# Kernel tuning notes

Measured on AMD Instinct MI355X. Metric: run time of the kernel, lower is better.

Reference implementation:

```python
import jax, jax.numpy as jnp
import numpy as np

N_GRAPHS = 50
EPS = 1e-5
N_NODES, N_EDGES, F, L, N_HEADS = 50000, 800000, 64, 3, 3


def _bn(x, gamma, beta):
    # BatchNorm1d over nodes, training-mode (biased batch statistics)
    m = x.mean(axis=0)
    v = jnp.mean((x - m) ** 2, axis=0)
    return gamma * (x - m) * jax.lax.rsqrt(v + EPS) + beta


def _pna_layer(x, src, dst, preW, preb, postW, postb, linW, linb, avg_log, avg_lin):
    N = x.shape[0]
    # pre-MLP on concatenated (target x_i, source x_j): [E, 2F] -> [E, F]
    h = jnp.concatenate([x[dst], x[src]], axis=-1) @ preW + preb
    ones = jnp.ones((h.shape[0],), h.dtype)
    cnt = jax.ops.segment_sum(ones, dst, num_segments=N)[:, None]
    has = cnt > 0
    deg = jnp.maximum(cnt, 1.0)  # PNAConv clamps degree to >= 1
    mean = jax.ops.segment_sum(h, dst, num_segments=N) / deg
    mean2 = jax.ops.segment_sum(h * h, dst, num_segments=N) / deg
    std = jnp.sqrt(jax.nn.relu(mean2 - mean * mean) + EPS)
    mn = jnp.where(has, jax.ops.segment_min(h, dst, num_segments=N), 0.0)
    mx = jnp.where(has, jax.ops.segment_max(h, dst, num_segments=N), 0.0)
    aggr = jnp.concatenate([mean, mn, mx, std], axis=-1)  # [N, 4F]
    log_deg = jnp.log(deg + 1.0)
    out = jnp.concatenate([aggr,
                           aggr * (log_deg / avg_log),   # amplification
                           aggr * (avg_log / log_deg),   # attenuation
                           aggr * (deg / avg_lin)],      # linear
                          axis=-1)                       # [N, 16F]
    out = jnp.concatenate([x, out], axis=-1) @ postW + postb  # post-MLP [N, F]
    return out @ linW + linb


def _forward(x, deg_hist, preW, preb, postW, postb, linW, linb, bn_g, bn_b,
             sharedW, sharedb, hW1, hb1, hW2, hb2, hW3, hb3, src, dst, batch):
    bins = jnp.arange(deg_hist.shape[0], dtype=deg_hist.dtype)
    tot = deg_hist.sum()
    avg_lin = (bins * deg_hist).sum() / tot
    avg_log = (jnp.log(bins + 1.0) * deg_hist).sum() / tot
    for l in range(preW.shape[0]):  # only num_conv_layers convs run (zip truncation)
        x = _pna_layer(x, src, dst, preW[l], preb[l], postW[l], postb[l],
                       linW[l], linb[l], avg_log, avg_lin)
        x = jax.nn.relu(_bn(x, bn_g[l], bn_b[l]))
    gcnt = jax.ops.segment_sum(jnp.ones((x.shape[0],), x.dtype), batch,
                               num_segments=N_GRAPHS)[:, None]
    g = jax.ops.segment_sum(x, batch, num_segments=N_GRAPHS) / jnp.maximum(gcnt, 1.0)
    g = jax.nn.relu(g @ sharedW + sharedb)  # shared MLP (num_shared=1)
    h1 = jax.nn.relu(jnp.einsum('gd,hdk->hgk', g, hW1) + hb1[:, None, :])
    h2 = jax.nn.relu(jnp.einsum('hgk,hkm->hgm', h1, hW2) + hb2[:, None, :])
    o = jnp.einsum('hgm,hmo->hgo', h2, hW3) + hb3[:, None, :]  # [H, G, 1]
    return jnp.transpose(o[..., 0])  # [G, H] == torch.cat(head outputs, dim=1)


def setup_inputs():
    key = jax.random.key(0)
    ks = jax.random.split(key, 12)

    def w(k, shape, fan_in):
        return jax.random.normal(k, shape, jnp.float32) / np.sqrt(fan_in)

    return {
        "x": jax.random.normal(ks[0], (N_NODES, F), jnp.float32),
        "edge_index": jax.random.randint(ks[1], (2, N_EDGES), 0, N_NODES),
        "batch": jnp.sort(jax.random.randint(ks[2], (N_NODES,), 0, N_GRAPHS)),
        "deg_hist": jax.random.uniform(ks[3], (33,), jnp.float32) + 0.01,
        "preW": w(ks[4], (L, 2 * F, F), 2 * F),
        "preb": jnp.zeros((L, F), jnp.float32),
        "postW": w(ks[5], (L, 17 * F, F), 17 * F),
        "postb": jnp.zeros((L, F), jnp.float32),
        "linW": w(ks[6], (L, F, F), F),
        "linb": jnp.zeros((L, F), jnp.float32),
        "bn_g": jnp.ones((L, F), jnp.float32),
        "bn_b": jnp.zeros((L, F), jnp.float32),
        "sharedW": w(ks[7], (F, F), F),
        "sharedb": jnp.zeros((F,), jnp.float32),
        "hW1": w(ks[8], (N_HEADS, F, 50), F),
        "hb1": jnp.zeros((N_HEADS, 50), jnp.float32),
        "hW2": w(ks[9], (N_HEADS, 50, 25), 50),
        "hb2": jnp.zeros((N_HEADS, 25), jnp.float32),
        "hW3": w(ks[10], (N_HEADS, 25, 1), 25),
        "hb3": jnp.zeros((N_HEADS, 1), jnp.float32),
    }


def reference(x, edge_index, batch, deg_hist, preW, preb, postW, postb,
              linW, linb, bn_g, bn_b, sharedW, sharedb,
              hW1, hb1, hW2, hb2, hW3, hb3):
    return _forward(x, deg_hist, preW, preb, postW, postb, linW, linb,
                    bn_g, bn_b, sharedW, sharedb, hW1, hb1, hW2, hb2,
                    hW3, hb3, edge_index[0], edge_index[1], batch)
```

## Files before the change

### kernel.cpp

```cpp
#include <hip/hip_runtime.h>
#include <math.h>

#define N_NODES 50000
#define N_EDGES 800000
#define NGRAPHS 50
#define NHEADS 3
#define EPS 1e-5f
#define NPASS 8
#define PASS_W ((N_NODES + NPASS - 1) / NPASS)

typedef _Float16 half8 __attribute__((ext_vector_type(8)));
typedef float f32x4 __attribute__((ext_vector_type(4)));

__global__ void __launch_bounds__(256) k_zero_setup(int* cnt, int* cur, float* gsum, float* gcnt,
                                                    float* part, float* partq,
                                                    const float* dh, int nbins, float* scal) {
  int gid = blockIdx.x * 256 + threadIdx.x;
  int gs = gridDim.x * 256;
  for (int i = gid; i < N_NODES; i += gs) { cnt[i] = 0; cur[i] = 0; }
  for (int i = gid; i < NGRAPHS * 64; i += gs) gsum[i] = 0.f;
  for (int i = gid; i < NGRAPHS; i += gs) gcnt[i] = 0.f;
  for (int i = gid; i < 128 * 64; i += gs) { part[i] = 0.f; partq[i] = 0.f; }
  if (blockIdx.x == 0 && threadIdx.x < 64) {
    int t = threadIdx.x;
    float v = (t < nbins) ? dh[t] : 0.f;
    float lv = logf((float)t + 1.f) * v;
    float bv = (float)t * v;
    for (int d = 32; d > 0; d >>= 1) {
      v  += __shfl_down(v,  d, 64);
      lv += __shfl_down(lv, d, 64);
      bv += __shfl_down(bv, d, 64);
    }
    if (t == 0) { scal[0] = lv / v; scal[1] = bv / v; }
  }
}

__global__ void __launch_bounds__(256) k_hist(const int* __restrict__ dst, int* __restrict__ cnt) {
  int e = blockIdx.x * 256 + threadIdx.x;
  if (e < N_EDGES) atomicAdd(&cnt[dst[e]], 1);
}

__global__ void __launch_bounds__(256) k_scan_a(const int* __restrict__ cnt, int* __restrict__ off,
                                                int* __restrict__ blksum) {
  __shared__ int lds[256];
  int t = threadIdx.x;
  int base = blockIdx.x * 1024 + t * 4;
  int v0 = (base + 0 < N_NODES) ? cnt[base + 0] : 0;
  int v1 = (base + 1 < N_NODES) ? cnt[base + 1] : 0;
  int v2 = (base + 2 < N_NODES) ? cnt[base + 2] : 0;
  int v3 = (base + 3 < N_NODES) ? cnt[base + 3] : 0;
  int tsum = v0 + v1 + v2 + v3;
  lds[t] = tsum; __syncthreads();
  for (int d = 1; d < 256; d <<= 1) {
    int x = (t >= d) ? lds[t - d] : 0;
    __syncthreads();
    lds[t] += x;
    __syncthreads();
  }
  int run = lds[t] - tsum;
  if (base + 0 < N_NODES) off[base + 0] = run; run += v0;
  if (base + 1 < N_NODES) off[base + 1] = run; run += v1;
  if (base + 2 < N_NODES) off[base + 2] = run; run += v2;
  if (base + 3 < N_NODES) off[base + 3] = run;
  if (t == 255) blksum[blockIdx.x] = lds[255];
}

__global__ void __launch_bounds__(64) k_scan_b(const int* __restrict__ blksum, int* __restrict__ blkoff) {
  int t = threadIdx.x;
  int own = (t < 49) ? blksum[t] : 0;
  int v = own;
  for (int d = 1; d < 64; d <<= 1) {
    int u = __shfl_up(v, d, 64);
    if (t >= d) v += u;
  }
  if (t < 49) blkoff[t] = v - own;
}

__global__ void __launch_bounds__(256) k_scan_c(int* __restrict__ off, const int* __restrict__ blkoff) {
  int i = blockIdx.x * 256 + threadIdx.x;
  if (i < N_NODES) off[i] += blkoff[i >> 10];
  if (i == 0) off[N_NODES] = N_EDGES;
}

__global__ void __launch_bounds__(256) k_scatter(const int* __restrict__ src, const int* __restrict__ dst,
                                                 const int* __restrict__ off, int* __restrict__ cur,
                                                 int* __restrict__ esrc) {
  int e = blockIdx.x * 256 + threadIdx.x;
  if (e >= N_EDGES) return;
  int d = dst[e];
  int sv = src[e] << 7;
  #pragma unroll 1
  for (int p = 0; p < NPASS; ++p) {
    int lo = p * PASS_W;
    if (d >= lo && d < lo + PASS_W) {
      int pos = off[d] + atomicAdd(&cur[d], 1);
      esrc[pos] = sv;
    }
  }
}

__global__ void __launch_bounds__(256) k_prep(const float* __restrict__ xin, _Float16* __restrict__ xout,
                                              const float* __restrict__ preW, const float* __restrict__ postW,
                                              const float* __restrict__ linW, _Float16* __restrict__ preP,
                                              _Float16* __restrict__ postAP, _Float16* __restrict__ postBP,
                                              _Float16* __restrict__ linP) {
  int t0 = blockIdx.x * 256 + threadIdx.x;
  if (t0 < 400000) {
    const float* s = xin + (size_t)t0 * 8;
    float4 v0 = *(const float4*)s;
    float4 v1 = *(const float4*)(s + 4);
    half8 h = {(_Float16)v0.x, (_Float16)v0.y, (_Float16)v0.z, (_Float16)v0.w,
               (_Float16)v1.x, (_Float16)v1.y, (_Float16)v1.z, (_Float16)v1.w};
    *(half8*)(xout + (size_t)t0 * 8) = h;
    return;
  }
  int t = t0 - 400000;
  if (t < 24576) {
    int l = t >> 13, r = t & 8191;
    int j = r & 7, lane = (r >> 3) & 63, ctg = (r >> 9) & 7, kc = r >> 12;
    int k = kc * 32 + ((lane >> 4) << 3) + j;
    int col = ctg * 16 + (lane & 15);
    const float* W = preW + (size_t)l * 8192;
    float v = (col < 64) ? W[k * 64 + col] : W[(64 + k) * 64 + (col - 64)];
    preP[(size_t)l * 8192 + r] = (_Float16)v;
  } else if (t < 221184) {
    int q = t - 24576;
    int l = q >> 16, r = q & 65535;
    int j = r & 7, lane = (r >> 3) & 63, ct = (r >> 9) & 3, s = (r >> 11) & 3, kc = r >> 13;
    int k = kc * 32 + ((lane >> 4) << 3) + j;
    int col = ct * 16 + (lane & 15);
    postAP[(size_t)l * 65536 + r] = (_Float16)postW[(size_t)l * 69632 + (size_t)(64 + s * 256 + k) * 64 + col];
  } else if (t < 233472) {
    int q = t - 221184;
    int l = q >> 12, r = q & 4095;
    int j = r & 7, lane = (r >> 3) & 63, ct = (r >> 9) & 3, kc = r >> 11;
    int k = kc * 32 + ((lane >> 4) << 3) + j;
    int col = ct * 16 + (lane & 15);
    postBP[(size_t)l * 4096 + r] = (_Float16)postW[(size_t)l * 69632 + (size_t)k * 64 + col];
  } else if (t < 245760) {
    int q = t - 233472;
    int l = q >> 12, r = q & 4095;
    int j = r & 7, lane = (r >> 3) & 63, ct = (r >> 9) & 3, kc = r >> 11;
    int k = kc * 32 + ((lane >> 4) << 3) + j;
    int col = ct * 16 + (lane & 15);
    linP[(size_t)l * 4096 + r] = (_Float16)linW[(size_t)l * 4096 + (size_t)k * 64 + col];
  }
}

__global__ void __launch_bounds__(256) k_mfma_g1(const _Float16* __restrict__ yin, const float* __restrict__ bnsc,
                                                 const float* __restrict__ bnsh, int applyBN,
                                                 const _Float16* __restrict__ wp, const float* __restrict__ bias,
                                                 _Float16* __restrict__ Aout, _Float16* __restrict__ Bout,
                                                 _Float16* __restrict__ xout) {
  int t = threadIdx.x, lane = t & 63, wave = t >> 6;
  int r0 = blockIdx.x * 64;
  int mrow = lane & 15, q8 = ((lane >> 4) << 3);
  f32x4 acc[4][2];
  #pragma unroll
  for (int rt = 0; rt < 4; ++rt) { acc[rt][0] = (f32x4)0.f; acc[rt][1] = (f32x4)0.f; }
  #pragma unroll
  for (int kc = 0; kc < 2; ++kc) {
    int k0 = kc * 32 + q8;
    half8 a[4];
    #pragma unroll
    for (int rt = 0; rt < 4; ++rt) {
      int r = min(r0 + rt * 16 + mrow, N_NODES - 1);
      a[rt] = *(const half8*)(yin + (size_t)r * 64 + k0);
    }
    if (applyBN) {
      float4 sc0 = *(const float4*)(bnsc + k0);
      float4 sc1 = *(const float4*)(bnsc + k0 + 4);
      float4 sh0 = *(const float4*)(bnsh + k0);
      float4 sh1 = *(const float4*)(bnsh + k0 + 4);
      #pragma unroll
      for (int rt = 0; rt < 4; ++rt) {
        half8 v = a[rt];
        v[0] = (_Float16)fmaxf((float)v[0] * sc0.x + sh0.x, 0.f);
        v[1] = (_Float16)fmaxf((float)v[1] * sc0.y + sh0.y, 0.f);
        v[2] = (_Float16)fmaxf((float)v[2] * sc0.z + sh0.z, 0.f);
        v[3] = (_Float16)fmaxf((float)v[3] * sc0.w + sh0.w, 0.f);
        v[4] = (_Float16)fmaxf((float)v[4] * sc1.x + sh1.x, 0.f);
        v[5] = (_Float16)fmaxf((float)v[5] * sc1.y + sh1.y, 0.f);
        v[6] = (_Float16)fmaxf((float)v[6] * sc1.z + sh1.z, 0.f);
        v[7] = (_Float16)fmaxf((float)v[7] * sc1.w + sh1.w, 0.f);
        a[rt] = v;
      }
      if (wave == 0) {
        #pragma unroll
        for (int rt = 0; rt < 4; ++rt) {
          int r = min(r0 + rt * 16 + mrow, N_NODES - 1);
          *(half8*)(xout + (size_t)r * 64 + k0) = a[rt];
        }
      }
    }
    #pragma unroll
    for (int ci = 0; ci < 2; ++ci) {
      int ctg = wave * 2 + ci;
      half8 b = *(const half8*)(wp + (size_t)((kc * 8 + ctg) * 64 + lane) * 8);
      #pragma unroll
      for (int rt = 0; rt < 4; ++rt)
        acc[rt][ci] = __builtin_amdgcn_mfma_f32_16x16x32_f16(a[rt], b, acc[rt][ci], 0, 0, 0);
    }
  }
  #pragma unroll
  for (int ci = 0; ci < 2; ++ci) {
    int col = (wave * 2 + ci) * 16 + mrow;
    bool isA = col < 64;
    float bv = isA ? bias[col] : 0.f;
    _Float16* outp = isA ? (Aout + col) : (Bout + (col - 64));
    #pragma unroll
    for (int rt = 0; rt < 4; ++rt)
      #pragma unroll
      for (int reg = 0; reg < 4; ++reg) {
        int row = r0 + rt * 16 + ((lane >> 4) << 2) + reg;
        if (row < N_NODES) outp[(size_t)row * 64] = (_Float16)(acc[rt][ci][reg] + bv);
      }
  }
}

__global__ void __launch_bounds__(256) k_aggr(const _Float16* __restrict__ A, const _Float16* __restrict__ B,
                                              const int* __restrict__ off, const int* __restrict__ esrc,
                                              const float* __restrict__ scal, _Float16* __restrict__ aggr,
                                              float4* __restrict__ scales) {
  int wave = threadIdx.x >> 6, lane = threadIdx.x & 63;
  int n = blockIdx.x * 4 + wave;
  float c = (float)A[(size_t)n * 64 + lane];
  int e0 = __builtin_amdgcn_readfirstlane(off[n]);
  int e1 = __builtin_amdgcn_readfirstlane(off[n + 1]);
  int deg = e1 - e0;
  const char* Bb = (const char*)B;
  int lo2 = lane * 2;
  float sum = 0.f, sq = 0.f, mn = 3.4e38f, mx = -3.4e38f;
  int e = e0;
  for (; e + 3 < e1; e += 4) {
    int r0 = __builtin_amdgcn_readfirstlane(esrc[e]);
    int r1 = __builtin_amdgcn_readfirstlane(esrc[e + 1]);
    int r2 = __builtin_amdgcn_readfirstlane(esrc[e + 2]);
    int r3 = __builtin_amdgcn_readfirstlane(esrc[e + 3]);
    float b0 = (float)*(const _Float16*)(Bb + r0 + lo2);
    float b1 = (float)*(const _Float16*)(Bb + r1 + lo2);
    float b2 = (float)*(const _Float16*)(Bb + r2 + lo2);
    float b3 = (float)*(const _Float16*)(Bb + r3 + lo2);
    sum += (b0 + b1) + (b2 + b3);
    sq += b0 * b0; sq += b1 * b1; sq += b2 * b2; sq += b3 * b3;
    mn = fminf(mn, fminf(fminf(b0, b1), fminf(b2, b3)));
    mx = fmaxf(mx, fmaxf(fmaxf(b0, b1), fmaxf(b2, b3)));
  }
  for (; e < e1; ++e) {
    int r = __builtin_amdgcn_readfirstlane(esrc[e]);
    float b = (float)*(const _Float16*)(Bb + r + lo2);
    sum += b; sq += b * b; mn = fminf(mn, b); mx = fmaxf(mx, b);
  }
  _Float16* arow = aggr + (size_t)n * 256;
  if (deg == 0) {
    arow[lane] = (_Float16)0.f; arow[64 + lane] = (_Float16)0.f;
    arow[128 + lane] = (_Float16)0.f; arow[192 + lane] = (_Float16)sqrtf(EPS);
  } else {
    float inv = 1.f / (float)deg;
    float mb = sum * inv, m2 = sq * inv;
    float var = fmaxf(m2 - mb * mb, 0.f);
    arow[lane]       = (_Float16)(c + mb);
    arow[64 + lane]  = (_Float16)(c + mn);
    arow[128 + lane] = (_Float16)(c + mx);
    arow[192 + lane] = (_Float16)sqrtf(var + EPS);
  }
  if (lane == 0) {
    float degf = fmaxf((float)deg, 1.f);
    float ld = logf(degf + 1.f);
    float al = scal[0], av = scal[1];
    scales[n] = make_float4(ld / al, al / ld, degf / av, 0.f);
  }
}

__global__ void __launch_bounds__(256) k_mfma_g2(const _Float16* __restrict__ aggr, const _Float16* __restrict__ x16,
                                                 const _Float16* __restrict__ wpA, const _Float16* __restrict__ wpB,
                                                 const float* __restrict__ postb, const float4* __restrict__ scales,
                                                 _Float16* __restrict__ ybuf) {
  int t = threadIdx.x, lane = t & 63, ct = t >> 6;
  int r0 = blockIdx.x * 64;
  int mrow = lane & 15, q8 = ((lane >> 4) << 3);
  f32x4 acc[4][4];
  #pragma unroll
  for (int rt = 0; rt < 4; ++rt)
    #pragma unroll
    for (int s = 0; s < 4; ++s) acc[rt][s] = (f32x4)0.f;
  #pragma unroll 2
  for (int kc = 0; kc < 8; ++kc) {
    half8 a[4];
    #pragma unroll
    for (int rt = 0; rt < 4; ++rt) {
      int r = min(r0 + rt * 16 + mrow, N_NODES - 1);
      a[rt] = *(const half8*)(aggr + (size_t)r * 256 + kc * 32 + q8);
    }
    #pragma unroll
    for (int s = 0; s < 4; ++s) {
      half8 b = *(const half8*)(wpA + (size_t)((((kc * 4 + s) * 4 + ct) * 64) + lane) * 8);
      #pragma unroll
      for (int rt = 0; rt < 4; ++rt)
        acc[rt][s] = __builtin_amdgcn_mfma_f32_16x16x32_f16(a[rt], b, acc[rt][s], 0, 0, 0);
    }
  }
  #pragma unroll
  for (int kc = 0; kc < 2; ++kc) {
    half8 a[4];
    #pragma unroll
    for (int rt = 0; rt < 4; ++rt) {
      int r = min(r0 + rt * 16 + mrow, N_NODES - 1);
      a[rt] = *(const half8*)(x16 + (size_t)r * 64 + kc * 32 + q8);
    }
    half8 b = *(const half8*)(wpB + (size_t)(((kc * 4 + ct) * 64) + lane) * 8);
    #pragma unroll
    for (int rt = 0; rt < 4; ++rt)
      acc[rt][0] = __builtin_amdgcn_mfma_f32_16x16x32_f16(a[rt], b, acc[rt][0], 0, 0, 0);
  }
  int col = ct * 16 + mrow;
  float pb = postb[col];
  #pragma unroll
  for (int rt = 0; rt < 4; ++rt)
    #pragma unroll
    for (int reg = 0; reg < 4; ++reg) {
      int row = r0 + rt * 16 + ((lane >> 4) << 2) + reg;
      if (row < N_NODES) {
        float4 sc = scales[row];
        float v = acc[rt][0][reg] + sc.x * acc[rt][1][reg] + sc.y * acc[rt][2][reg] + sc.z * acc[rt][3][reg] + pb;
        ybuf[(size_t)row * 64 + col] = (_Float16)v;
      }
    }
}

__global__ void __launch_bounds__(256) k_mfma_g3(const _Float16* __restrict__ yin, const _Float16* __restrict__ wp,
                                                 const float* __restrict__ bias, _Float16* __restrict__ y16,
                                                 float* __restrict__ part, float* __restrict__ partq) {
  int t = threadIdx.x, lane = t & 63, ct = t >> 6;
  int r0 = blockIdx.x * 64;
  int mrow = lane & 15, q8 = ((lane >> 4) << 3);
  f32x4 acc[4];
  #pragma unroll
  for (int rt = 0; rt < 4; ++rt) acc[rt] = (f32x4)0.f;
  #pragma unroll
  for (int kc = 0; kc < 2; ++kc) {
    half8 a[4];
    #pragma unroll
    for (int rt = 0; rt < 4; ++rt) {
      int r = min(r0 + rt * 16 + mrow, N_NODES - 1);
      a[rt] = *(const half8*)(yin + (size_t)r * 64 + kc * 32 + q8);
    }
    half8 b = *(const half8*)(wp + (size_t)(((kc * 4 + ct) * 64) + lane) * 8);
    #pragma unroll
    for (int rt = 0; rt < 4; ++rt)
      acc[rt] = __builtin_amdgcn_mfma_f32_16x16x32_f16(a[rt], b, acc[rt], 0, 0, 0);
  }
  int col = ct * 16 + mrow;
  float bv = bias[col];
  float s = 0.f, q = 0.f;
  #pragma unroll
  for (int rt = 0; rt < 4; ++rt)
    #pragma unroll
    for (int reg = 0; reg < 4; ++reg) {
      int row = r0 + rt * 16 + ((lane >> 4) << 2) + reg;
      if (row < N_NODES) {
        float v = acc[rt][reg] + bv;
        y16[(size_t)row * 64 + col] = (_Float16)v;
        s += v; q += v * v;
      }
    }
  int slot = (blockIdx.x & 127) * 64 + col;
  atomicAdd(&part[slot], s);
  atomicAdd(&partq[slot], q);
}

__global__ void __launch_bounds__(256) k_bnfinal(float* __restrict__ part, float* __restrict__ partq,
                                                 const float* __restrict__ g, const float* __restrict__ b,
                                                 float* __restrict__ scale, float* __restrict__ shift) {
  __shared__ float ls[256], lq[256];
  int t = threadIdx.x, col = t & 63, qtr = t >> 6;
  float s = 0.f, q = 0.f;
  for (int i = 0; i < 32; ++i) {
    int slot = qtr * 32 + i;
    s += part[slot * 64 + col];
    q += partq[slot * 64 + col];
  }
  ls[t] = s; lq[t] = q; __syncthreads();
  if (t < 64) {
    s = ls[t] + ls[64 + t] + ls[128 + t] + ls[192 + t];
    q = lq[t] + lq[64 + t] + lq[128 + t] + lq[192 + t];
    float m = s / (float)N_NODES;
    float v = fmaxf(q / (float)N_NODES - m * m, 0.f);
    float sc = g[t] * rsqrtf(v + EPS);
    scale[t] = sc;
    shift[t] = b[t] - m * sc;
  }
  __syncthreads();
  for (int i = t; i < 128 * 64; i += 256) { part[i] = 0.f; partq[i] = 0.f; }
}

__global__ void __launch_bounds__(256) k_pool(const _Float16* __restrict__ y16, const float* __restrict__ bnsc,
                                              const float* __restrict__ bnsh, const int* __restrict__ batch,
                                              float* __restrict__ gsum, float* __restrict__ gcnt) {
  int t = threadIdx.x, col = t & 63, rl = t >> 6;
  float sc = bnsc[col], sh = bnsh[col];
  int rbeg = blockIdx.x * 64 + rl * 16;
  int rend = min(rbeg + 16, N_NODES);
  int curg = -1, cr = 0;
  float acc = 0.f;
  for (int r = rbeg; r < rend; ++r) {
    int g = batch[r];
    if (g != curg) {
      if (curg >= 0) {
        atomicAdd(&gsum[curg * 64 + col], acc);
        if (col == 0) atomicAdd(&gcnt[curg], (float)cr);
      }
      curg = g; acc = 0.f; cr = 0;
    }
    acc += fmaxf((float)y16[(size_t)r * 64 + col] * sc + sh, 0.f); cr++;
  }
  if (curg >= 0) {
    atomicAdd(&gsum[curg * 64 + col], acc);
    if (col == 0) atomicAdd(&gcnt[curg], (float)cr);
  }
}

__global__ void __launch_bounds__(64) k_shared(const float* __restrict__ gsum, const float* __restrict__ gcnt,
                                               const float* __restrict__ W, const float* __restrict__ b,
                                               float* __restrict__ g2) {
  __shared__ float gm[64];
  int g = blockIdx.x, j = threadIdx.x;
  float cv = fmaxf(gcnt[g], 1.f);
  gm[j] = gsum[g * 64 + j] / cv;
  __syncthreads();
  float s = b[j];
  for (int k = 0; k < 64; ++k) s += gm[k] * W[k * 64 + j];
  g2[g * 64 + j] = fmaxf(s, 0.f);
}

__global__ void __launch_bounds__(64) k_heads(const float* __restrict__ g2, const float* __restrict__ hW1,
                                              const float* __restrict__ hb1, const float* __restrict__ hW2,
                                              const float* __restrict__ hb2, const float* __restrict__ hW3,
                                              const float* __restrict__ hb3, float* __restrict__ out) {
  __shared__ float gv[64], h1[50], h2[25];
  int bid = blockIdx.x;
  int g = bid / NHEADS, h = bid % NHEADS;
  int t = threadIdx.x;
  gv[t] = g2[g * 64 + t];
  __syncthreads();
  if (t < 50) {
    float s = hb1[h * 50 + t];
    for (int k = 0; k < 64; ++k) s += gv[k] * hW1[h * 3200 + k * 50 + t];
    h1[t] = fmaxf(s, 0.f);
  }
  __syncthreads();
  if (t < 25) {
    float s = hb2[h * 25 + t];
    for (int k = 0; k < 50; ++k) s += h1[k] * hW2[h * 1250 + k * 25 + t];
    h2[t] = fmaxf(s, 0.f);
  }
  __syncthreads();
  if (t == 0) {
    float s = hb3[h];
    for (int k = 0; k < 25; ++k) s += h2[k] * hW3[h * 25 + k];
    out[g * NHEADS + h] = s;
  }
}

extern "C" void kernel_launch(void* const* d_in, const int* in_sizes, int n_in,
                              void* d_out, int out_size, void* d_ws, size_t ws_size,
                              hipStream_t stream) {
  const float* x0    = (const float*)d_in[0];
  const int*   eidx  = (const int*)d_in[1];
  const int*   batch = (const int*)d_in[2];
  const float* dh    = (const float*)d_in[3];
  const float* preW  = (const float*)d_in[4];
  const float* preb  = (const float*)d_in[5];
  const float* postW = (const float*)d_in[6];
  const float* postb = (const float*)d_in[7];
  const float* linW  = (const float*)d_in[8];
  const float* linb  = (const float*)d_in[9];
  const float* bng   = (const float*)d_in[10];
  const float* bnb   = (const float*)d_in[11];
  const float* shW   = (const float*)d_in[12];
  const float* shb   = (const float*)d_in[13];
  const float* hW1   = (const float*)d_in[14];
  const float* hb1   = (const float*)d_in[15];
  const float* hW2   = (const float*)d_in[16];
  const float* hb2   = (const float*)d_in[17];
  const float* hW3   = (const float*)d_in[18];
  const float* hb3   = (const float*)d_in[19];
  float* out = (float*)d_out;

  char* ws = (char*)d_ws;
  size_t o = 0;
  auto alloc = [&](size_t bytes) {
    char* p = ws + o;
    o = (o + bytes + 255) & ~(size_t)255;
    return p;
  };
  float* scal   = (float*)alloc(8 * 4);
  int* off      = (int*)alloc((N_NODES + 1) * 4);
  int* cnt      = (int*)alloc(N_NODES * 4);
  int* cur      = (int*)alloc(N_NODES * 4);
  int* esrc     = (int*)alloc(N_EDGES * 4);
  int* blks     = (int*)alloc(64 * 4);
  int* blko     = (int*)alloc(64 * 4);
  _Float16* A16    = (_Float16*)alloc((size_t)N_NODES * 64 * 2 + 256 * 16);
  _Float16* B16    = (_Float16*)alloc((size_t)N_NODES * 64 * 2 + 256 * 16);
  _Float16* aggr16 = (_Float16*)alloc((size_t)50048 * 256 * 2);
  _Float16* x16a   = (_Float16*)alloc((size_t)N_NODES * 64 * 2 + 256 * 16);
  _Float16* xbuf   = (_Float16*)alloc((size_t)N_NODES * 64 * 2 + 256 * 16);
  _Float16* ybuf16 = (_Float16*)alloc((size_t)N_NODES * 64 * 2 + 256 * 16);
  _Float16* y16    = (_Float16*)alloc((size_t)N_NODES * 64 * 2 + 256 * 16);
  float4* scales = (float4*)alloc((size_t)N_NODES * 16);
  _Float16* preP   = (_Float16*)alloc(3 * 8192 * 2);
  _Float16* postAP = (_Float16*)alloc((size_t)3 * 65536 * 2);
  _Float16* postBP = (_Float16*)alloc(3 * 4096 * 2);
  _Float16* linP   = (_Float16*)alloc(3 * 4096 * 2);
  float* part   = (float*)alloc(128 * 64 * 4);
  float* partq  = (float*)alloc(128 * 64 * 4);
  float* bnsc   = (float*)alloc(64 * 4);
  float* bnsh   = (float*)alloc(64 * 4);
  float* gsum   = (float*)alloc(NGRAPHS * 64 * 4);
  float* gcnt   = (float*)alloc(NGRAPHS * 4);
  float* g2b    = (float*)alloc(NGRAPHS * 64 * 4);

  const int* srcv = eidx;
  const int* dstv = eidx + N_EDGES;

  k_zero_setup<<<256, 256, 0, stream>>>(cnt, cur, gsum, gcnt, part, partq, dh, in_sizes[3], scal);
  k_hist<<<(N_EDGES + 255) / 256, 256, 0, stream>>>(dstv, cnt);
  k_scan_a<<<49, 256, 0, stream>>>(cnt, off, blks);
  k_scan_b<<<1, 64, 0, stream>>>(blks, blko);
  k_scan_c<<<196, 256, 0, stream>>>(off, blko);
  k_scatter<<<(N_EDGES + 255) / 256, 256, 0, stream>>>(srcv, dstv, off, cur, esrc);
  k_prep<<<(400000 + 245760 + 255) / 256, 256, 0, stream>>>(x0, x16a, preW, postW, linW,
                                                            preP, postAP, postBP, linP);

  for (int l = 0; l < 3; ++l) {
    const _Float16* g1in = (l == 0) ? x16a : y16;
    const _Float16* xc   = (l == 0) ? x16a : xbuf;
    k_mfma_g1<<<782, 256, 0, stream>>>(g1in, bnsc, bnsh, (l > 0) ? 1 : 0,
                                       preP + (size_t)l * 8192, preb + l * 64, A16, B16, xbuf);
    k_aggr<<<12500, 256, 0, stream>>>(A16, B16, off, esrc, scal, aggr16, scales);
    k_mfma_g2<<<782, 256, 0, stream>>>(aggr16, xc, postAP + (size_t)l * 65536, postBP + (size_t)l * 4096,
                                       postb + l * 64, scales, ybuf16);
    k_mfma_g3<<<782, 256, 0, stream>>>(ybuf16, linP + (size_t)l * 4096, linb + l * 64, y16, part, partq);
    k_bnfinal<<<1, 256, 0, stream>>>(part, partq, bng + l * 64, bnb + l * 64, bnsc, bnsh);
  }
  k_pool<<<782, 256, 0, stream>>>(y16, bnsc, bnsh, batch, gsum, gcnt);
  k_shared<<<NGRAPHS, 64, 0, stream>>>(gsum, gcnt, shW, shb, g2b);
  k_heads<<<NGRAPHS * NHEADS, 64, 0, stream>>>(g2b, hW1, hb1, hW2, hb2, hW3, hb3, out);
}
```

Measured before the change: 501.8 us.

## Fuse aggregation into post-MLP GEMM, two-level CSR partition, merge head kernels

Three changes land together. The edge-to-CSR scatter, which used 8 passes of global atomics, becomes a two-stage partition: edges are first binned into 256-node windows through per-block shared-memory histograms, then each window is sorted locally in LDS before being written out. The per-node aggregation kernel is fused into the post-MLP MFMA kernel, so the aggregate rows and degree scalers stay in shared memory and never round-trip through global memory. The shared-MLP and head kernels are merged into one launch. The cost is fewer aggregation waves in flight (782 blocks, each wave handling 16 nodes serially instead of one node per wave) and extra workspace for the partition buffers.

```diff
diff --git a/kernel.cpp b/kernel.cpp
--- a/kernel.cpp
+++ b/kernel.cpp
@@ -6,18 +6,18 @@
 #define NGRAPHS 50
 #define NHEADS 3
 #define EPS 1e-5f
-#define NPASS 8
-#define PASS_W ((N_NODES + NPASS - 1) / NPASS)
+#define NWIN 196
+#define WSH 8
 
 typedef _Float16 half8 __attribute__((ext_vector_type(8)));
 typedef float f32x4 __attribute__((ext_vector_type(4)));
 
-__global__ void __launch_bounds__(256) k_zero_setup(int* cnt, int* cur, float* gsum, float* gcnt,
+__global__ void __launch_bounds__(256) k_zero_setup(int* cnt, float* gsum, float* gcnt,
                                                     float* part, float* partq,
                                                     const float* dh, int nbins, float* scal) {
   int gid = blockIdx.x * 256 + threadIdx.x;
   int gs = gridDim.x * 256;
-  for (int i = gid; i < N_NODES; i += gs) { cnt[i] = 0; cur[i] = 0; }
+  for (int i = gid; i < N_NODES; i += gs) cnt[i] = 0;
   for (int i = gid; i < NGRAPHS * 64; i += gs) gsum[i] = 0.f;
   for (int i = gid; i < NGRAPHS; i += gs) gcnt[i] = 0.f;
   for (int i = gid; i < 128 * 64; i += gs) { part[i] = 0.f; partq[i] = 0.f; }
@@ -76,25 +76,102 @@
   if (t < 49) blkoff[t] = v - own;
 }
 
-__global__ void __launch_bounds__(256) k_scan_c(int* __restrict__ off, const int* __restrict__ blkoff) {
+__global__ void __launch_bounds__(256) k_scan_c(int* __restrict__ off, const int* __restrict__ blkoff,
+                                                int* __restrict__ wincur) {
   int i = blockIdx.x * 256 + threadIdx.x;
-  if (i < N_NODES) off[i] += blkoff[i >> 10];
+  if (i < N_NODES) {
+    int fo = off[i] + blkoff[i >> 10];
+    off[i] = fo;
+    if ((i & 255) == 0) wincur[i >> WSH] = fo;
+  }
   if (i == 0) off[N_NODES] = N_EDGES;
 }
 
-__global__ void __launch_bounds__(256) k_scatter(const int* __restrict__ src, const int* __restrict__ dst,
-                                                 const int* __restrict__ off, int* __restrict__ cur,
-                                                 int* __restrict__ esrc) {
-  int e = blockIdx.x * 256 + threadIdx.x;
-  if (e >= N_EDGES) return;
-  int d = dst[e];
-  int sv = src[e] << 7;
-  #pragma unroll 1
-  for (int p = 0; p < NPASS; ++p) {
-    int lo = p * PASS_W;
-    if (d >= lo && d < lo + PASS_W) {
-      int pos = off[d] + atomicAdd(&cur[d], 1);
-      esrc[pos] = sv;
+__global__ void __launch_bounds__(256) k_part1(const int* __restrict__ src, const int* __restrict__ dst,
+                                               int* __restrict__ wincur, int* __restrict__ pairS,
+                                               unsigned char* __restrict__ pairDL) {
+  __shared__ int hist[256];
+  __shared__ int scan[256];
+  __shared__ int baseg[256];
+  __shared__ int place[256];
+  __shared__ int sS[2048];
+  __shared__ unsigned char sDL[2048];
+  __shared__ unsigned char sW[2048];
+  int t = threadIdx.x;
+  int base = blockIdx.x * 2048;
+  hist[t] = 0;
+  __syncthreads();
+  int d[8], s[8];
+  #pragma unroll
+  for (int i = 0; i < 8; ++i) {
+    int e = base + t + 256 * i;
+    bool val = e < N_EDGES;
+    d[i] = val ? dst[e] : -1;
+    s[i] = val ? src[e] : 0;
+    if (val) atomicAdd(&hist[d[i] >> WSH], 1);
+  }
+  __syncthreads();
+  int v = hist[t];
+  scan[t] = v; __syncthreads();
+  for (int dd = 1; dd < 256; dd <<= 1) {
+    int x = (t >= dd) ? scan[t - dd] : 0;
+    __syncthreads();
+    scan[t] += x;
+    __syncthreads();
+  }
+  place[t] = scan[t] - v;
+  if (v > 0) baseg[t] = atomicAdd(&wincur[t], v);
+  __syncthreads();
+  #pragma unroll
+  for (int i = 0; i < 8; ++i) {
+    if (d[i] >= 0) {
+      int w = d[i] >> WSH;
+      int p = atomicAdd(&place[w], 1);
+      sS[p] = s[i] << 7;
+      sDL[p] = (unsigned char)(d[i] & 255);
+      sW[p] = (unsigned char)w;
+    }
+  }
+  __syncthreads();
+  int tot = min(N_EDGES - base, 2048);
+  for (int i = t; i < tot; i += 256) {
+    int w = sW[i];
+    int gidx = baseg[w] + (i - (scan[w] - hist[w]));
+    pairS[gidx] = sS[i];
+    pairDL[gidx] = sDL[i];
+  }
+}
+
+__global__ void __launch_bounds__(256) k_part2(const int* __restrict__ off, const int* __restrict__ pairS,
+                                               const unsigned char* __restrict__ pairDL,
+                                               int* __restrict__ esrc) {
+  __shared__ int curW[256];
+  __shared__ int offW[257];
+  __shared__ int esrcW[6144];
+  int w = blockIdx.x, t = threadIdx.x;
+  int n0 = w << WSH;
+  offW[t] = off[min(n0 + t, N_NODES)];
+  if (t == 0) offW[256] = off[min(n0 + 256, N_NODES)];
+  curW[t] = 0;
+  __syncthreads();
+  int start = offW[0];
+  int end = offW[256];
+  int cnt = end - start;
+  if (cnt <= 6144) {
+    for (int i = t; i < cnt; i += 256) {
+      int s = pairS[start + i];
+      int dl = pairDL[start + i];
+      int pos = offW[dl] - start + atomicAdd(&curW[dl], 1);
+      esrcW[pos] = s;
+    }
+    __syncthreads();
+    for (int i = t; i < cnt; i += 256) esrc[start + i] = esrcW[i];
+  } else {
+    for (int i = t; i < cnt; i += 256) {
+      int s = pairS[start + i];
+      int dl = pairDL[start + i];
+      int pos = offW[dl] + atomicAdd(&curW[dl], 1);
+      esrc[pos] = s;
     }
   }
 }
@@ -218,66 +295,75 @@
   }
 }
 
-__global__ void __launch_bounds__(256) k_aggr(const _Float16* __restrict__ A, const _Float16* __restrict__ B,
-                                              const int* __restrict__ off, const int* __restrict__ esrc,
-                                              const float* __restrict__ scal, _Float16* __restrict__ aggr,
-                                              float4* __restrict__ scales) {
-  int wave = threadIdx.x >> 6, lane = threadIdx.x & 63;
-  int n = blockIdx.x * 4 + wave;
-  float c = (float)A[(size_t)n * 64 + lane];
-  int e0 = __builtin_amdgcn_readfirstlane(off[n]);
-  int e1 = __builtin_amdgcn_readfirstlane(off[n + 1]);
-  int deg = e1 - e0;
+__global__ void __launch_bounds__(256) k_aggr_g2(const _Float16* __restrict__ A, const _Float16* __restrict__ B,
+                                                 const int* __restrict__ off, const int* __restrict__ esrc,
+                                                 const float* __restrict__ scal, const _Float16* __restrict__ x16,
+                                                 const _Float16* __restrict__ wpA, const _Float16* __restrict__ wpB,
+                                                 const float* __restrict__ postb, _Float16* __restrict__ ybuf) {
+  __shared__ _Float16 aggrS[64][264];
+  __shared__ float sclS[64][4];
+  int t = threadIdx.x, lane = t & 63, wave = t >> 6;
+  int r0 = blockIdx.x * 64;
+  float al = scal[0], av = scal[1];
   const char* Bb = (const char*)B;
   int lo2 = lane * 2;
-  float sum = 0.f, sq = 0.f, mn = 3.4e38f, mx = -3.4e38f;
-  int e = e0;
-  for (; e + 3 < e1; e += 4) {
-    int r0 = __builtin_amdgcn_readfirstlane(esrc[e]);
-    int r1 = __builtin_amdgcn_readfirstlane(esrc[e + 1]);
-    int r2 = __builtin_amdgcn_readfirstlane(esrc[e + 2]);
-    int r3 = __builtin_amdgcn_readfirstlane(esrc[e + 3]);
-    float b0 = (float)*(const _Float16*)(Bb + r0 + lo2);
-    float b1 = (float)*(const _Float16*)(Bb + r1 + lo2);
-    float b2 = (float)*(const _Float16*)(Bb + r2 + lo2);
-    float b3 = (float)*(const _Float16*)(Bb + r3 + lo2);
-    sum += (b0 + b1) + (b2 + b3);
-    sq += b0 * b0; sq += b1 * b1; sq += b2 * b2; sq += b3 * b3;
-    mn = fminf(mn, fminf(fminf(b0, b1), fminf(b2, b3)));
-    mx = fmaxf(mx, fmaxf(fmaxf(b0, b1), fmaxf(b2, b3)));
-  }
-  for (; e < e1; ++e) {
-    int r = __builtin_amdgcn_readfirstlane(esrc[e]);
-    float b = (float)*(const _Float16*)(Bb + r + lo2);
-    sum += b; sq += b * b; mn = fminf(mn, b); mx = fmaxf(mx, b);
-  }
-  _Float16* arow = aggr + (size_t)n * 256;
-  if (deg == 0) {
-    arow[lane] = (_Float16)0.f; arow[64 + lane] = (_Float16)0.f;
-    arow[128 + lane] = (_Float16)0.f; arow[192 + lane] = (_Float16)sqrtf(EPS);
-  } else {
-    float inv = 1.f / (float)deg;
-    float mb = sum * inv, m2 = sq * inv;
-    float var = fmaxf(m2 - mb * mb, 0.f);
-    arow[lane]       = (_Float16)(c + mb);
-    arow[64 + lane]  = (_Float16)(c + mn);
-    arow[128 + lane] = (_Float16)(c + mx);
-    arow[192 + lane] = (_Float16)sqrtf(var + EPS);
-  }
-  if (lane == 0) {
-    float degf = fmaxf((float)deg, 1.f);
-    float ld = logf(degf + 1.f);
-    float al = scal[0], av = scal[1];
-    scales[n] = make_float4(ld / al, al / ld, degf / av, 0.f);
-  }
-}
-
-__global__ void __launch_bounds__(256) k_mfma_g2(const _Float16* __restrict__ aggr, const _Float16* __restrict__ x16,
-                                                 const _Float16* __restrict__ wpA, const _Float16* __restrict__ wpB,
-                                                 const float* __restrict__ postb, const float4* __restrict__ scales,
-                                                 _Float16* __restrict__ ybuf) {
-  int t = threadIdx.x, lane = t & 63, ct = t >> 6;
-  int r0 = blockIdx.x * 64;
+  for (int i = 0; i < 16; ++i) {
+    int nl = wave * 16 + i;
+    int n = r0 + nl;
+    float c = 0.f;
+    int e0 = 0, e1 = 0;
+    if (n < N_NODES) {
+      c = (float)A[(size_t)n * 64 + lane];
+      e0 = off[n]; e1 = off[n + 1];
+    }
+    e0 = __builtin_amdgcn_readfirstlane(e0);
+    e1 = __builtin_amdgcn_readfirstlane(e1);
+    int deg = e1 - e0;
+    float sum = 0.f, sq = 0.f, mn = 3.4e38f, mx = -3.4e38f;
+    int e = e0;
+    for (; e + 3 < e1; e += 4) {
+      int b0o = __builtin_amdgcn_readfirstlane(esrc[e]);
+      int b1o = __builtin_amdgcn_readfirstlane(esrc[e + 1]);
+      int b2o = __builtin_amdgcn_readfirstlane(esrc[e + 2]);
+      int b3o = __builtin_amdgcn_readfirstlane(esrc[e + 3]);
+      float b0 = (float)*(const _Float16*)(Bb + b0o + lo2);
+      float b1 = (float)*(const _Float16*)(Bb + b1o + lo2);
+      float b2 = (float)*(const _Float16*)(Bb + b2o + lo2);
+      float b3 = (float)*(const _Float16*)(Bb + b3o + lo2);
+      sum += (b0 + b1) + (b2 + b3);
+      sq += b0 * b0; sq += b1 * b1; sq += b2 * b2; sq += b3 * b3;
+      mn = fminf(mn, fminf(fminf(b0, b1), fminf(b2, b3)));
+      mx = fmaxf(mx, fmaxf(fmaxf(b0, b1), fmaxf(b2, b3)));
+    }
+    for (; e < e1; ++e) {
+      int ro = __builtin_amdgcn_readfirstlane(esrc[e]);
+      float b = (float)*(const _Float16*)(Bb + ro + lo2);
+      sum += b; sq += b * b; mn = fminf(mn, b); mx = fmaxf(mx, b);
+    }
+    if (deg == 0) {
+      aggrS[nl][lane] = (_Float16)0.f;
+      aggrS[nl][64 + lane] = (_Float16)0.f;
+      aggrS[nl][128 + lane] = (_Float16)0.f;
+      aggrS[nl][192 + lane] = (_Float16)sqrtf(EPS);
+    } else {
+      float inv = 1.f / (float)deg;
+      float mb = sum * inv, m2 = sq * inv;
+      float var = fmaxf(m2 - mb * mb, 0.f);
+      aggrS[nl][lane]       = (_Float16)(c + mb);
+      aggrS[nl][64 + lane]  = (_Float16)(c + mn);
+      aggrS[nl][128 + lane] = (_Float16)(c + mx);
+      aggrS[nl][192 + lane] = (_Float16)sqrtf(var + EPS);
+    }
+    if (lane == 0) {
+      float degf = fmaxf((float)deg, 1.f);
+      float ld = logf(degf + 1.f);
+      sclS[nl][0] = ld / al;
+      sclS[nl][1] = al / ld;
+      sclS[nl][2] = degf / av;
+    }
+  }
+  __syncthreads();
+  int ct = wave;
   int mrow = lane & 15, q8 = ((lane >> 4) << 3);
   f32x4 acc[4][4];
   #pragma unroll
@@ -288,10 +374,8 @@
   for (int kc = 0; kc < 8; ++kc) {
     half8 a[4];
     #pragma unroll
-    for (int rt = 0; rt < 4; ++rt) {
-      int r = min(r0 + rt * 16 + mrow, N_NODES - 1);
-      a[rt] = *(const half8*)(aggr + (size_t)r * 256 + kc * 32 + q8);
-    }
+    for (int rt = 0; rt < 4; ++rt)
+      a[rt] = *(const half8*)(&aggrS[rt * 16 + mrow][kc * 32 + q8]);
     #pragma unroll
     for (int s = 0; s < 4; ++s) {
       half8 b = *(const half8*)(wpA + (size_t)((((kc * 4 + s) * 4 + ct) * 64) + lane) * 8);
@@ -319,10 +403,11 @@
   for (int rt = 0; rt < 4; ++rt)
     #pragma unroll
     for (int reg = 0; reg < 4; ++reg) {
-      int row = r0 + rt * 16 + ((lane >> 4) << 2) + reg;
+      int rr = rt * 16 + ((lane >> 4) << 2) + reg;
+      int row = r0 + rr;
       if (row < N_NODES) {
-        float4 sc = scales[row];
-        float v = acc[rt][0][reg] + sc.x * acc[rt][1][reg] + sc.y * acc[rt][2][reg] + sc.z * acc[rt][3][reg] + pb;
+        float s1 = sclS[rr][0], s2 = sclS[rr][1], s3 = sclS[rr][2];
+        float v = acc[rt][0][reg] + s1 * acc[rt][1][reg] + s2 * acc[rt][2][reg] + s3 * acc[rt][3][reg] + pb;
         ybuf[(size_t)row * 64 + col] = (_Float16)v;
       }
     }
@@ -420,28 +505,22 @@
   }
 }
 
-__global__ void __launch_bounds__(64) k_shared(const float* __restrict__ gsum, const float* __restrict__ gcnt,
-                                               const float* __restrict__ W, const float* __restrict__ b,
-                                               float* __restrict__ g2) {
-  __shared__ float gm[64];
-  int g = blockIdx.x, j = threadIdx.x;
-  float cv = fmaxf(gcnt[g], 1.f);
-  gm[j] = gsum[g * 64 + j] / cv;
-  __syncthreads();
-  float s = b[j];
-  for (int k = 0; k < 64; ++k) s += gm[k] * W[k * 64 + j];
-  g2[g * 64 + j] = fmaxf(s, 0.f);
-}
-
-__global__ void __launch_bounds__(64) k_heads(const float* __restrict__ g2, const float* __restrict__ hW1,
-                                              const float* __restrict__ hb1, const float* __restrict__ hW2,
-                                              const float* __restrict__ hb2, const float* __restrict__ hW3,
-                                              const float* __restrict__ hb3, float* __restrict__ out) {
-  __shared__ float gv[64], h1[50], h2[25];
+__global__ void __launch_bounds__(64) k_sharedheads(const float* __restrict__ gsum, const float* __restrict__ gcnt,
+                                                    const float* __restrict__ W, const float* __restrict__ b,
+                                                    const float* __restrict__ hW1, const float* __restrict__ hb1,
+                                                    const float* __restrict__ hW2, const float* __restrict__ hb2,
+                                                    const float* __restrict__ hW3, const float* __restrict__ hb3,
+                                                    float* __restrict__ out) {
+  __shared__ float gm[64], gv[64], h1[50], h2[25];
   int bid = blockIdx.x;
   int g = bid / NHEADS, h = bid % NHEADS;
   int t = threadIdx.x;
-  gv[t] = g2[g * 64 + t];
+  float cv = fmaxf(gcnt[g], 1.f);
+  gm[t] = gsum[g * 64 + t] / cv;
+  __syncthreads();
+  float s0 = b[t];
+  for (int k = 0; k < 64; ++k) s0 += gm[k] * W[k * 64 + t];
+  gv[t] = fmaxf(s0, 0.f);
   __syncthreads();
   if (t < 50) {
     float s = hb1[h * 50 + t];
@@ -497,18 +576,18 @@
   float* scal   = (float*)alloc(8 * 4);
   int* off      = (int*)alloc((N_NODES + 1) * 4);
   int* cnt      = (int*)alloc(N_NODES * 4);
-  int* cur      = (int*)alloc(N_NODES * 4);
   int* esrc     = (int*)alloc(N_EDGES * 4);
+  int* pairS    = (int*)alloc(N_EDGES * 4);
+  unsigned char* pairDL = (unsigned char*)alloc(N_EDGES);
+  int* wincur   = (int*)alloc(NWIN * 4);
   int* blks     = (int*)alloc(64 * 4);
   int* blko     = (int*)alloc(64 * 4);
   _Float16* A16    = (_Float16*)alloc((size_t)N_NODES * 64 * 2 + 256 * 16);
   _Float16* B16    = (_Float16*)alloc((size_t)N_NODES * 64 * 2 + 256 * 16);
-  _Float16* aggr16 = (_Float16*)alloc((size_t)50048 * 256 * 2);
   _Float16* x16a   = (_Float16*)alloc((size_t)N_NODES * 64 * 2 + 256 * 16);
   _Float16* xbuf   = (_Float16*)alloc((size_t)N_NODES * 64 * 2 + 256 * 16);
   _Float16* ybuf16 = (_Float16*)alloc((size_t)N_NODES * 64 * 2 + 256 * 16);
   _Float16* y16    = (_Float16*)alloc((size_t)N_NODES * 64 * 2 + 256 * 16);
-  float4* scales = (float4*)alloc((size_t)N_NODES * 16);
   _Float16* preP   = (_Float16*)alloc(3 * 8192 * 2);
   _Float16* postAP = (_Float16*)alloc((size_t)3 * 65536 * 2);
   _Float16* postBP = (_Float16*)alloc(3 * 4096 * 2);
@@ -519,17 +598,17 @@
   float* bnsh   = (float*)alloc(64 * 4);
   float* gsum   = (float*)alloc(NGRAPHS * 64 * 4);
   float* gcnt   = (float*)alloc(NGRAPHS * 4);
-  float* g2b    = (float*)alloc(NGRAPHS * 64 * 4);
 
   const int* srcv = eidx;
   const int* dstv = eidx + N_EDGES;
 
-  k_zero_setup<<<256, 256, 0, stream>>>(cnt, cur, gsum, gcnt, part, partq, dh, in_sizes[3], scal);
+  k_zero_setup<<<256, 256, 0, stream>>>(cnt, gsum, gcnt, part, partq, dh, in_sizes[3], scal);
   k_hist<<<(N_EDGES + 255) / 256, 256, 0, stream>>>(dstv, cnt);
   k_scan_a<<<49, 256, 0, stream>>>(cnt, off, blks);
   k_scan_b<<<1, 64, 0, stream>>>(blks, blko);
-  k_scan_c<<<196, 256, 0, stream>>>(off, blko);
-  k_scatter<<<(N_EDGES + 255) / 256, 256, 0, stream>>>(srcv, dstv, off, cur, esrc);
+  k_scan_c<<<196, 256, 0, stream>>>(off, blko, wincur);
+  k_part1<<<(N_EDGES + 2047) / 2048, 256, 0, stream>>>(srcv, dstv, wincur, pairS, pairDL);
+  k_part2<<<NWIN, 256, 0, stream>>>(off, pairS, pairDL, esrc);
   k_prep<<<(400000 + 245760 + 255) / 256, 256, 0, stream>>>(x0, x16a, preW, postW, linW,
                                                             preP, postAP, postBP, linP);
 
@@ -538,13 +617,13 @@
     const _Float16* xc   = (l == 0) ? x16a : xbuf;
     k_mfma_g1<<<782, 256, 0, stream>>>(g1in, bnsc, bnsh, (l > 0) ? 1 : 0,
                                        preP + (size_t)l * 8192, preb + l * 64, A16, B16, xbuf);
-    k_aggr<<<12500, 256, 0, stream>>>(A16, B16, off, esrc, scal, aggr16, scales);
-    k_mfma_g2<<<782, 256, 0, stream>>>(aggr16, xc, postAP + (size_t)l * 65536, postBP + (size_t)l * 4096,
-                                       postb + l * 64, scales, ybuf16);
+    k_aggr_g2<<<782, 256, 0, stream>>>(A16, B16, off, esrc, scal, xc,
+                                       postAP + (size_t)l * 65536, postBP + (size_t)l * 4096,
+                                       postb + l * 64, ybuf16);
     k_mfma_g3<<<782, 256, 0, stream>>>(ybuf16, linP + (size_t)l * 4096, linb + l * 64, y16, part, partq);
     k_bnfinal<<<1, 256, 0, stream>>>(part, partq, bng + l * 64, bnb + l * 64, bnsc, bnsh);
   }
   k_pool<<<782, 256, 0, stream>>>(y16, bnsc, bnsh, batch, gsum, gcnt);
-  k_shared<<<NGRAPHS, 64, 0, stream>>>(gsum, gcnt, shW, shb, g2b);
-  k_heads<<<NGRAPHS * NHEADS, 64, 0, stream>>>(g2b, hW1, hb1, hW2, hb2, hW3, hb3, out);
-}
+  k_sharedheads<<<NGRAPHS * NHEADS, 64, 0, stream>>>(gsum, gcnt, shW, shb,
+                                                     hW1, hb1, hW2, hb2, hW3, hb3, out);
+}
```

Measured after the change: 612.5 us. 22.0% more time.
